# Performance work log

Hardware: AMD Instinct MI355X
Metric: run time of the kernel (lower is better)

Reference implementation:

```python
import jax, jax.numpy as jnp
import numpy as np

W, H = 256, 256          # image width (x) and height (y); image indexed [x, y] like the torch code
N = 8192                 # depth-sorted visible gaussians
TILE = 16                # tile_size default
CHUNK = 128              # gaussians composited per scan step (N % CHUNK == 0)
MIN_WEIGHT = 1e-6        # early-termination threshold from render_pixel


def setup_inputs() -> dict:
    key = jax.random.key(0)
    k1, k2, k3, k4, k5 = jax.random.split(key, 5)
    # pixel-space means, uniformly over the image
    points_xy = jax.random.uniform(k1, (N, 2), dtype=jnp.float32) * jnp.array([W, H], jnp.float32)
    # SPD inverse 2D covariances: Sigma = R diag(var) R^T, inv = R diag(1/var) R^T
    theta = jax.random.uniform(k2, (N,), dtype=jnp.float32) * (2.0 * np.pi)
    sig = jax.random.uniform(k3, (N, 2), dtype=jnp.float32, minval=1.5, maxval=8.0)
    var = sig ** 2
    ct, st = jnp.cos(theta), jnp.sin(theta)
    R = jnp.stack([jnp.stack([ct, -st], -1), jnp.stack([st, ct], -1)], -2)  # [N,2,2]
    inverse_covariance = jnp.einsum('nij,nj,nkj->nik', R, 1.0 / var, R)
    # radius = ceil(2.5 * sqrt(max eigenvalue)) as in compute_radius
    radius = jnp.ceil(2.5 * jnp.sqrt(jnp.max(var, axis=1)))
    colors = jax.random.uniform(k4, (N, 3), dtype=jnp.float32)
    opacity = jax.random.normal(k5, (N,), dtype=jnp.float32)  # pre-sigmoid logits
    return dict(points_xy=points_xy, inverse_covariance=inverse_covariance,
                radius=radius, colors=colors, opacity=opacity)


def _rasterize(points_xy, inverse_covariance, radius, colors, opacity):
    px = jnp.arange(W, dtype=jnp.float32)[:, None]   # [W,1] pixel x coords
    py = jnp.arange(H, dtype=jnp.float32)[None, :]   # [1,H] pixel y coords
    # tile origin for each pixel (tile-based culling as in render_image)
    tile_x0 = ((jnp.arange(W) // TILE) * TILE).astype(jnp.float32)[:, None]  # [W,1]
    tile_y0 = ((jnp.arange(H) // TILE) * TILE).astype(jnp.float32)[None, :]  # [1,H]
    # per-gaussian bounding boxes (preprocess)
    min_x = jnp.floor(points_xy[:, 0] - radius); max_x = jnp.ceil(points_xy[:, 0] + radius)
    min_y = jnp.floor(points_xy[:, 1] - radius); max_y = jnp.ceil(points_xy[:, 1] + radius)

    n_chunks = N // CHUNK
    def chunk(a):
        return a.reshape((n_chunks, CHUNK) + a.shape[1:])
    xs = dict(mx=chunk(points_xy[:, 0]), my=chunk(points_xy[:, 1]),
              a=chunk(inverse_covariance[:, 0, 0]), b=chunk(inverse_covariance[:, 0, 1]),
              c=chunk(inverse_covariance[:, 1, 1]),
              mnx=chunk(min_x), mxx=chunk(max_x), mny=chunk(min_y), mxy=chunk(max_y),
              col=chunk(colors), op=chunk(opacity))

    @jax.checkpoint
    def body(carry, ch):
        T, color = carry  # T: [W,H] remaining transmittance; color: [W,H,3]
        dx = px[None] - ch['mx'][:, None, None]  # [C,W,1]
        dy = py[None] - ch['my'][:, None, None]  # [C,1,H]
        # mahalanobis form d^T Sigma^{-1} d with symmetric inv cov [[a,b],[b,c]]
        q = (ch['a'][:, None, None] * dx * dx
             + 2.0 * ch['b'][:, None, None] * dx * dy
             + ch['c'][:, None, None] * dy * dy)              # [C,W,H]
        alpha = jnp.exp(-0.5 * q) * jax.nn.sigmoid(ch['op'])[:, None, None]
        # gaussian participates for a pixel iff its bbox intersects that pixel's tile
        in_tile = ((ch['mnx'][:, None, None] <= tile_x0[None] + TILE)
                   & (ch['mxx'][:, None, None] >= tile_x0[None])
                   & (ch['mny'][:, None, None] <= tile_y0[None] + TILE)
                   & (ch['mxy'][:, None, None] >= tile_y0[None]))   # [C,W,H]
        alpha = jnp.where(in_tile, alpha, 0.0)
        cum = jnp.cumprod(1.0 - alpha, axis=0)                 # inclusive prefix of (1-alpha)
        T_before = T[None] * jnp.concatenate([jnp.ones_like(cum[:1]), cum[:-1]], axis=0)
        # original: test_weight = T_before*(1-alpha); terminate (skip contribution) if < min_weight
        include = (T[None] * cum) >= MIN_WEIGHT
        contrib = jnp.where(include, T_before * alpha, 0.0)   # [C,W,H]
        color = color + jnp.einsum('cwh,cd->whd', contrib, ch['col'])
        return (T * cum[-1], color), None

    init = (jnp.ones((W, H), jnp.float32), jnp.zeros((W, H, 3), jnp.float32))
    (_, color), _ = jax.lax.scan(body, init, xs)
    return color  # [W,H,3] image indexed [x,y]


def reference(points_xy, inverse_covariance, radius, colors, opacity):
    return _rasterize(points_xy, inverse_covariance, radius, colors, opacity)
```

## Files before the change

### kernel.cpp

```cpp
#include <hip/hip_runtime.h>
#include <hip/hip_fp16.h>

#define WIDTH   256
#define HEIGHT  256
#define NG      8192
#define TILE_SZ 16
#define MINW    1e-6f
#define BLK     1024
#define NBATCH  (NG / BLK)
#define NWAVE   (BLK / 64)
#define NSEG    8
#define PXB     128
#define RSZ     1024

__global__ __launch_bounds__(BLK, 8) void raster_kernel(
    const float* __restrict__ pts,
    const float* __restrict__ icov,
    const float* __restrict__ rad,
    const float* __restrict__ cols,
    const float* __restrict__ opac,
    float* __restrict__ out)
{
    __shared__ unsigned long long s_ball[NBATCH * NWAVE];
    __shared__ int s_pfx[NBATCH * NWAVE];
    __shared__ unsigned short s_list[NG];
    __shared__ float4 s_g[RSZ * 2];
    __shared__ float s_P[NSEG][PXB];
    __shared__ float s_red[NSEG][PXB][3];

    const int tid  = threadIdx.x;
    const int lane = tid & 63;
    const int wave = tid >> 6;
    const int seg  = tid >> 7;
    const int pxl  = tid & (PXB - 1);
    const int px   = blockIdx.z * PXB + pxl;
    const float tx0 = (float)(blockIdx.x * TILE_SZ);
    const float ty0 = (float)(blockIdx.y * TILE_SZ);
    const float tx1 = tx0 + (float)TILE_SZ;
    const float ty1 = ty0 + (float)TILE_SZ;

    unsigned int hitbits = 0;
    for (int b = 0; b < NBATCH; ++b) {
        const int g = b * BLK + tid;
        const float2 p = ((const float2*)pts)[g];
        const float  r = rad[g];
        bool hit = (floorf(p.x - r) <= tx1) & (ceilf(p.x + r) >= tx0)
                 & (floorf(p.y - r) <= ty1) & (ceilf(p.y + r) >= ty0);
        unsigned long long m = __ballot(hit);
        if (lane == 0) s_ball[b * NWAVE + wave] = m;
        if (hit) hitbits |= (1u << b);
    }
    __syncthreads();
    if (wave == 0) {
        int v0 = __popcll(s_ball[lane]);
        int v1 = __popcll(s_ball[64 + lane]);
        #pragma unroll
        for (int d = 1; d < 64; d <<= 1) {
            const int t0 = __shfl_up(v0, d);
            const int t1 = __shfl_up(v1, d);
            if (lane >= d) { v0 += t0; v1 += t1; }
        }
        s_pfx[lane] = v0;
        s_pfx[64 + lane] = v1 + __shfl(v0, 63);
    }
    __syncthreads();
    const int count = s_pfx[127];
    {
        unsigned int hb = hitbits;
        const unsigned long long ltmask = (1ull << lane) - 1ull;
        while (hb) {
            const int b = __ffs(hb) - 1;  hb &= hb - 1;
            const int idx = b * NWAVE + wave;
            const unsigned long long m = s_ball[idx];
            const int bs = idx ? s_pfx[idx - 1] : 0;
            s_list[bs + __popcll(m & ltmask)] = (unsigned short)(b * BLK + tid);
        }
    }
    __syncthreads();

    const float fx = tx0 + (float)(px >> 4);
    const float fy = ty0 + (float)(px & 15);
    const float kc = -0.72134752044f;
    float T = 1.0f, accr = 0.0f, accg = 0.0f, accb = 0.0f;

    for (int base = 0; base < count; base += RSZ) {
        const int n = min(RSZ, count - base);
        if (tid < n) {
            const int g = s_list[base + tid];
            const float2 p = ((const float2*)pts)[g];
            const float4 ic = ((const float4*)icov)[g];
            const float op = 1.0f / (1.0f + __expf(-opac[g]));
            const __half2 h = __floats2half2_rn(cols[3 * g], cols[3 * g + 1]);
            unsigned rgbits; __builtin_memcpy(&rgbits, &h, 4);
            s_g[tid * 2 + 0] = make_float4(p.x, p.y, kc * ic.x, 2.0f * kc * ic.y);
            s_g[tid * 2 + 1] = make_float4(kc * ic.w, op, __uint_as_float(rgbits),
                                           cols[3 * g + 2]);
        }
        __syncthreads();

        const int L = (n + NSEG - 1) >> 3;
        const int i0 = seg * L;
        const int i1 = min(i0 + L, n);

        float P = 1.0f, lr = 0.0f, lg = 0.0f, lb = 0.0f;
        if (__ballot(T >= MINW) != 0ull) {
            #pragma unroll 4
            for (int i = i0; i < i1; ++i) {
                const float4 g0 = s_g[i * 2 + 0];
                const float4 g1 = s_g[i * 2 + 1];
                const float dx = fx - g0.x, dy = fy - g0.y;
                const float q = (g0.z * dx) * dx + (g0.w * dx) * dy + (g1.x * dy) * dy;
                const float a = g1.y * __builtin_amdgcn_exp2f(q);
                const float w = P * a;
                const unsigned rgbits = __float_as_uint(g1.z);
                __half2 h; __builtin_memcpy(&h, &rgbits, 4);
                const float2 rg = __half22float2(h);
                lr = fmaf(w, rg.x, lr);
                lg = fmaf(w, rg.y, lg);
                lb = fmaf(w, g1.w, lb);
                P = fmaf(-a, P, P);
            }
        }
        s_P[seg][pxl] = P;
        __syncthreads();

        float pv[NSEG];
        #pragma unroll
        for (int s = 0; s < NSEG; ++s) pv[s] = s_P[s][pxl];
        float Tin = T, Tnext = T;
        #pragma unroll
        for (int s = 0; s < NSEG; ++s) {
            if (s < seg) Tin *= pv[s];
            Tnext *= pv[s];
        }

        const bool alive = (Tin >= MINW);
        const bool gated = alive && (Tin * P < MINW);
        if (alive && !gated) {
            accr = fmaf(Tin, lr, accr);
            accg = fmaf(Tin, lg, accg);
            accb = fmaf(Tin, lb, accb);
        }
        if (__ballot(gated) != 0ull) {
            float Tl = Tin;
            for (int i = i0; i < i1; ++i) {
                const float4 g0 = s_g[i * 2 + 0];
                const float4 g1 = s_g[i * 2 + 1];
                const float dx = fx - g0.x, dy = fy - g0.y;
                const float q = (g0.z * dx) * dx + (g0.w * dx) * dy + (g1.x * dy) * dy;
                const float a = g1.y * __builtin_amdgcn_exp2f(q);
                const float Tn = Tl * (1.0f - a);
                const float w = (gated && Tn >= MINW) ? Tl * a : 0.0f;
                const unsigned rgbits = __float_as_uint(g1.z);
                __half2 h; __builtin_memcpy(&h, &rgbits, 4);
                const float2 rg = __half22float2(h);
                accr = fmaf(w, rg.x, accr);
                accg = fmaf(w, rg.y, accg);
                accb = fmaf(w, g1.w, accb);
                Tl = Tn;
            }
        }
        T = Tnext;
        if (__syncthreads_count(T < MINW) == BLK) break;
    }

    s_red[seg][pxl][0] = accr;
    s_red[seg][pxl][1] = accg;
    s_red[seg][pxl][2] = accb;
    __syncthreads();
    if (tid < PXB * 3) {
        const int p  = tid / 3;
        const int ch = tid - 3 * p;
        float v = 0.0f;
        #pragma unroll
        for (int s = 0; s < NSEG; ++s) v += s_red[s][p][ch];
        const int pg = blockIdx.z * PXB + p;
        const int x = blockIdx.x * TILE_SZ + (pg >> 4);
        const int y = blockIdx.y * TILE_SZ + (pg & 15);
        out[(x * HEIGHT + y) * 3 + ch] = v;
    }
}

extern "C" void kernel_launch(void* const* d_in, const int* in_sizes, int n_in,
                              void* d_out, int out_size, void* d_ws, size_t ws_size,
                              hipStream_t stream) {
    const float* pts  = (const float*)d_in[0];
    const float* icov = (const float*)d_in[1];
    const float* rad  = (const float*)d_in[2];
    const float* cols = (const float*)d_in[3];
    const float* opac = (const float*)d_in[4];
    float* out = (float*)d_out;
    dim3 grid(WIDTH / TILE_SZ, HEIGHT / TILE_SZ, 2);
    raster_kernel<<<grid, dim3(BLK), 0, stream>>>(pts, icov, rad, cols, opac, out);
}
```

Before: 84.82 us.

## Process two pixels per thread and split gaussians into sixteen segments

Each thread now shades two pixels (four rows apart) per gaussian loaded from shared memory, sharing the dy-dependent terms and the color unpack. The block is therefore split into 16 gaussian segments of one wave each instead of 8 segments of 128 threads. The reduction buffer now aliases the gaussian staging buffer to save LDS. This is meant to halve the shared-memory loads per pixel-gaussian evaluation and reuse the y-terms, at the cost of more registers per thread and a longer serial prefix combine over 16 segments.

```diff
diff --git a/kernel.cpp b/kernel.cpp
--- a/kernel.cpp
+++ b/kernel.cpp
@@ -9,7 +9,7 @@
 #define BLK     1024
 #define NBATCH  (NG / BLK)
 #define NWAVE   (BLK / 64)
-#define NSEG    8
+#define NSEG    16
 #define PXB     128
 #define RSZ     1024
 
@@ -26,14 +26,13 @@
     __shared__ unsigned short s_list[NG];
     __shared__ float4 s_g[RSZ * 2];
     __shared__ float s_P[NSEG][PXB];
-    __shared__ float s_red[NSEG][PXB][3];
+    float* s_red = (float*)s_g;
 
     const int tid  = threadIdx.x;
     const int lane = tid & 63;
     const int wave = tid >> 6;
-    const int seg  = tid >> 7;
-    const int pxl  = tid & (PXB - 1);
-    const int px   = blockIdx.z * PXB + pxl;
+    const int seg  = tid >> 6;
+    const int pair = tid & 63;
     const float tx0 = (float)(blockIdx.x * TILE_SZ);
     const float ty0 = (float)(blockIdx.y * TILE_SZ);
     const float tx1 = tx0 + (float)TILE_SZ;
@@ -78,10 +77,14 @@
     }
     __syncthreads();
 
-    const float fx = tx0 + (float)(px >> 4);
-    const float fy = ty0 + (float)(px & 15);
+    const int pA = pair;
+    const int pB = pair + 64;
+    const float fy  = ty0 + (float)(pair & 15);
+    const float fxA = tx0 + (float)(blockIdx.z * 8 + (pair >> 4));
+    const float fxB = fxA + 4.0f;
     const float kc = -0.72134752044f;
-    float T = 1.0f, accr = 0.0f, accg = 0.0f, accb = 0.0f;
+    float TA = 1.0f, TB = 1.0f;
+    float arA = 0.f, agA = 0.f, abA = 0.f, arB = 0.f, agB = 0.f, abB = 0.f;
 
     for (int base = 0; base < count; base += RSZ) {
         const int n = min(RSZ, count - base);
@@ -98,85 +101,109 @@
         }
         __syncthreads();
 
-        const int L = (n + NSEG - 1) >> 3;
+        const int L  = (n + NSEG - 1) >> 4;
         const int i0 = seg * L;
         const int i1 = min(i0 + L, n);
 
-        float P = 1.0f, lr = 0.0f, lg = 0.0f, lb = 0.0f;
-        if (__ballot(T >= MINW) != 0ull) {
+        float PA = 1.0f, PB = 1.0f;
+        float lrA = 0.f, lgA = 0.f, lbA = 0.f, lrB = 0.f, lgB = 0.f, lbB = 0.f;
+        if (__ballot((TA >= MINW) || (TB >= MINW)) != 0ull) {
             #pragma unroll 4
             for (int i = i0; i < i1; ++i) {
                 const float4 g0 = s_g[i * 2 + 0];
                 const float4 g1 = s_g[i * 2 + 1];
-                const float dx = fx - g0.x, dy = fy - g0.y;
-                const float q = (g0.z * dx) * dx + (g0.w * dx) * dy + (g1.x * dy) * dy;
-                const float a = g1.y * __builtin_amdgcn_exp2f(q);
-                const float w = P * a;
+                const float dy    = fy - g0.y;
+                const float bdy   = g0.w * dy;
+                const float cdydy = (g1.x * dy) * dy;
                 const unsigned rgbits = __float_as_uint(g1.z);
                 __half2 h; __builtin_memcpy(&h, &rgbits, 4);
                 const float2 rg = __half22float2(h);
-                lr = fmaf(w, rg.x, lr);
-                lg = fmaf(w, rg.y, lg);
-                lb = fmaf(w, g1.w, lb);
-                P = fmaf(-a, P, P);
+                const float dxA = fxA - g0.x;
+                const float qA  = fmaf(fmaf(g0.z, dxA, bdy), dxA, cdydy);
+                const float aA  = g1.y * __builtin_amdgcn_exp2f(qA);
+                const float wA  = PA * aA;
+                lrA = fmaf(wA, rg.x, lrA);
+                lgA = fmaf(wA, rg.y, lgA);
+                lbA = fmaf(wA, g1.w, lbA);
+                PA  = fmaf(-aA, PA, PA);
+                const float dxB = fxB - g0.x;
+                const float qB  = fmaf(fmaf(g0.z, dxB, bdy), dxB, cdydy);
+                const float aB  = g1.y * __builtin_amdgcn_exp2f(qB);
+                const float wB  = PB * aB;
+                lrB = fmaf(wB, rg.x, lrB);
+                lgB = fmaf(wB, rg.y, lgB);
+                lbB = fmaf(wB, g1.w, lbB);
+                PB  = fmaf(-aB, PB, PB);
             }
         }
-        s_P[seg][pxl] = P;
+        s_P[seg][pA] = PA;
+        s_P[seg][pB] = PB;
         __syncthreads();
 
-        float pv[NSEG];
-        #pragma unroll
-        for (int s = 0; s < NSEG; ++s) pv[s] = s_P[s][pxl];
-        float Tin = T, Tnext = T;
+        float TinA = TA, TnxA = TA, TinB = TB, TnxB = TB;
         #pragma unroll
         for (int s = 0; s < NSEG; ++s) {
-            if (s < seg) Tin *= pv[s];
-            Tnext *= pv[s];
-        }
-
-        const bool alive = (Tin >= MINW);
-        const bool gated = alive && (Tin * P < MINW);
-        if (alive && !gated) {
-            accr = fmaf(Tin, lr, accr);
-            accg = fmaf(Tin, lg, accg);
-            accb = fmaf(Tin, lb, accb);
-        }
-        if (__ballot(gated) != 0ull) {
-            float Tl = Tin;
+            const float vA = s_P[s][pA];
+            const float vB = s_P[s][pB];
+            if (s < seg) { TinA *= vA; TinB *= vB; }
+            TnxA *= vA;  TnxB *= vB;
+        }
+
+        const bool aliveA = (TinA >= MINW), aliveB = (TinB >= MINW);
+        const bool gatedA = aliveA && (TinA * PA < MINW);
+        const bool gatedB = aliveB && (TinB * PB < MINW);
+        if (aliveA && !gatedA) {
+            arA = fmaf(TinA, lrA, arA); agA = fmaf(TinA, lgA, agA); abA = fmaf(TinA, lbA, abA);
+        }
+        if (aliveB && !gatedB) {
+            arB = fmaf(TinB, lrB, arB); agB = fmaf(TinB, lgB, agB); abB = fmaf(TinB, lbB, abB);
+        }
+        if (__ballot(gatedA || gatedB) != 0ull) {
+            float TlA = TinA, TlB = TinB;
             for (int i = i0; i < i1; ++i) {
                 const float4 g0 = s_g[i * 2 + 0];
                 const float4 g1 = s_g[i * 2 + 1];
-                const float dx = fx - g0.x, dy = fy - g0.y;
-                const float q = (g0.z * dx) * dx + (g0.w * dx) * dy + (g1.x * dy) * dy;
-                const float a = g1.y * __builtin_amdgcn_exp2f(q);
-                const float Tn = Tl * (1.0f - a);
-                const float w = (gated && Tn >= MINW) ? Tl * a : 0.0f;
+                const float dy    = fy - g0.y;
+                const float bdy   = g0.w * dy;
+                const float cdydy = (g1.x * dy) * dy;
                 const unsigned rgbits = __float_as_uint(g1.z);
                 __half2 h; __builtin_memcpy(&h, &rgbits, 4);
                 const float2 rg = __half22float2(h);
-                accr = fmaf(w, rg.x, accr);
-                accg = fmaf(w, rg.y, accg);
-                accb = fmaf(w, g1.w, accb);
-                Tl = Tn;
+                const float dxA = fxA - g0.x;
+                const float aA  = g1.y * __builtin_amdgcn_exp2f(
+                                      fmaf(fmaf(g0.z, dxA, bdy), dxA, cdydy));
+                const float TnA = TlA * (1.0f - aA);
+                const float wA  = (gatedA && TnA >= MINW) ? TlA * aA : 0.0f;
+                arA = fmaf(wA, rg.x, arA); agA = fmaf(wA, rg.y, agA); abA = fmaf(wA, g1.w, abA);
+                TlA = TnA;
+                const float dxB = fxB - g0.x;
+                const float aB  = g1.y * __builtin_amdgcn_exp2f(
+                                      fmaf(fmaf(g0.z, dxB, bdy), dxB, cdydy));
+                const float TnB = TlB * (1.0f - aB);
+                const float wB  = (gatedB && TnB >= MINW) ? TlB * aB : 0.0f;
+                arB = fmaf(wB, rg.x, arB); agB = fmaf(wB, rg.y, agB); abB = fmaf(wB, g1.w, abB);
+                TlB = TnB;
             }
         }
-        T = Tnext;
-        if (__syncthreads_count(T < MINW) == BLK) break;
-    }
-
-    s_red[seg][pxl][0] = accr;
-    s_red[seg][pxl][1] = accg;
-    s_red[seg][pxl][2] = accb;
+        TA = TnxA;  TB = TnxB;
+        if (__syncthreads_count((TA < MINW) && (TB < MINW)) == BLK) break;
+    }
+
+    s_red[seg * (PXB * 3) + pA * 3 + 0] = arA;
+    s_red[seg * (PXB * 3) + pA * 3 + 1] = agA;
+    s_red[seg * (PXB * 3) + pA * 3 + 2] = abA;
+    s_red[seg * (PXB * 3) + pB * 3 + 0] = arB;
+    s_red[seg * (PXB * 3) + pB * 3 + 1] = agB;
+    s_red[seg * (PXB * 3) + pB * 3 + 2] = abB;
     __syncthreads();
     if (tid < PXB * 3) {
+        float v = 0.0f;
+        #pragma unroll
+        for (int s = 0; s < NSEG; ++s) v += s_red[s * (PXB * 3) + tid];
         const int p  = tid / 3;
         const int ch = tid - 3 * p;
-        float v = 0.0f;
-        #pragma unroll
-        for (int s = 0; s < NSEG; ++s) v += s_red[s][p][ch];
-        const int pg = blockIdx.z * PXB + p;
-        const int x = blockIdx.x * TILE_SZ + (pg >> 4);
-        const int y = blockIdx.y * TILE_SZ + (pg & 15);
+        const int x = blockIdx.x * TILE_SZ + blockIdx.z * 8 + (p >> 4);
+        const int y = blockIdx.y * TILE_SZ + (p & 15);
         out[(x * HEIGHT + y) * 3 + ch] = v;
     }
 }
```

After: 83.05 us. 1.02x faster.

## Shrink gaussian staging batch, alias shared buffers, centralize transmittance scan

Applied to the files above, without the earlier changes.

Halves the staging batch to 512 gaussians and aliases the index list, gaussian buffer and reduction buffer into one shared pool to reduce LDS footprint. The per-thread cross-segment transmittance product is replaced by a serial scan done by 128 threads that writes each segment's entry transmittance back to shared memory, at the cost of an extra barrier per batch. The warp-level early-skip ballot on the main loop is removed and the early-exit check now runs only on the first 128 threads. The quadratic form is also rewritten with nested fmas.

```diff
diff --git a/kernel.cpp b/kernel.cpp
--- a/kernel.cpp
+++ b/kernel.cpp
@@ -11,7 +11,8 @@
 #define NWAVE   (BLK / 64)
 #define NSEG    8
 #define PXB     128
-#define RSZ     1024
+#define RSZ     512
+#define KC      (-0.72134752044f)
 
 __global__ __launch_bounds__(BLK, 8) void raster_kernel(
     const float* __restrict__ pts,
@@ -23,23 +24,24 @@
 {
     __shared__ unsigned long long s_ball[NBATCH * NWAVE];
     __shared__ int s_pfx[NBATCH * NWAVE];
-    __shared__ unsigned short s_list[NG];
-    __shared__ float4 s_g[RSZ * 2];
+    __shared__ __align__(16) char s_pool[32768];
+    unsigned short* s_list = (unsigned short*)s_pool;
+    float4* s_g = (float4*)(s_pool + 16384);
+    float*  s_red = (float*)s_pool;
     __shared__ float s_P[NSEG][PXB];
-    __shared__ float s_red[NSEG][PXB][3];
 
     const int tid  = threadIdx.x;
     const int lane = tid & 63;
     const int wave = tid >> 6;
     const int seg  = tid >> 7;
-    const int pxl  = tid & (PXB - 1);
-    const int px   = blockIdx.z * PXB + pxl;
+    const int px   = tid & (PXB - 1);
     const float tx0 = (float)(blockIdx.x * TILE_SZ);
     const float ty0 = (float)(blockIdx.y * TILE_SZ);
     const float tx1 = tx0 + (float)TILE_SZ;
     const float ty1 = ty0 + (float)TILE_SZ;
 
     unsigned int hitbits = 0;
+    #pragma unroll
     for (int b = 0; b < NBATCH; ++b) {
         const int g = b * BLK + tid;
         const float2 p = ((const float2*)pts)[g];
@@ -78,10 +80,10 @@
     }
     __syncthreads();
 
-    const float fx = tx0 + (float)(px >> 4);
+    const float fx = tx0 + (float)(blockIdx.z * 8 + (px >> 4));
     const float fy = ty0 + (float)(px & 15);
-    const float kc = -0.72134752044f;
-    float T = 1.0f, accr = 0.0f, accg = 0.0f, accb = 0.0f;
+    float Tpx = 1.0f;
+    float ar = 0.f, ag = 0.f, ab = 0.f;
 
     for (int base = 0; base < count; base += RSZ) {
         const int n = min(RSZ, count - base);
@@ -92,91 +94,98 @@
             const float op = 1.0f / (1.0f + __expf(-opac[g]));
             const __half2 h = __floats2half2_rn(cols[3 * g], cols[3 * g + 1]);
             unsigned rgbits; __builtin_memcpy(&rgbits, &h, 4);
-            s_g[tid * 2 + 0] = make_float4(p.x, p.y, kc * ic.x, 2.0f * kc * ic.y);
-            s_g[tid * 2 + 1] = make_float4(kc * ic.w, op, __uint_as_float(rgbits),
+            s_g[tid * 2 + 0] = make_float4(p.x, p.y, KC * ic.x, 2.0f * KC * ic.y);
+            s_g[tid * 2 + 1] = make_float4(KC * ic.w, op, __uint_as_float(rgbits),
                                            cols[3 * g + 2]);
         }
         __syncthreads();
 
-        const int L = (n + NSEG - 1) >> 3;
+        const int L  = (n + NSEG - 1) >> 3;
         const int i0 = seg * L;
         const int i1 = min(i0 + L, n);
 
-        float P = 1.0f, lr = 0.0f, lg = 0.0f, lb = 0.0f;
-        if (__ballot(T >= MINW) != 0ull) {
-            #pragma unroll 4
-            for (int i = i0; i < i1; ++i) {
-                const float4 g0 = s_g[i * 2 + 0];
-                const float4 g1 = s_g[i * 2 + 1];
-                const float dx = fx - g0.x, dy = fy - g0.y;
-                const float q = (g0.z * dx) * dx + (g0.w * dx) * dy + (g1.x * dy) * dy;
-                const float a = g1.y * __builtin_amdgcn_exp2f(q);
-                const float w = P * a;
-                const unsigned rgbits = __float_as_uint(g1.z);
-                __half2 h; __builtin_memcpy(&h, &rgbits, 4);
-                const float2 rg = __half22float2(h);
-                lr = fmaf(w, rg.x, lr);
-                lg = fmaf(w, rg.y, lg);
-                lb = fmaf(w, g1.w, lb);
-                P = fmaf(-a, P, P);
+        float P = 1.0f, lr = 0.f, lg = 0.f, lb = 0.f;
+        #pragma unroll 4
+        for (int i = i0; i < i1; ++i) {
+            const float4 g0 = s_g[i * 2 + 0];
+            const float4 g1 = s_g[i * 2 + 1];
+            const float dx = fx - g0.x;
+            const float dy = fy - g0.y;
+            const float q  = fmaf(dx, fmaf(g0.z, dx, g0.w * dy),
+                                  (g1.x * dy) * dy);
+            const float a  = g1.y * __builtin_amdgcn_exp2f(q);
+            const float w  = P * a;
+            const unsigned rgbits = __float_as_uint(g1.z);
+            __half2 h; __builtin_memcpy(&h, &rgbits, 4);
+            const float2 rg = __half22float2(h);
+            lr = fmaf(w, rg.x, lr);
+            lg = fmaf(w, rg.y, lg);
+            lb = fmaf(w, g1.w, lb);
+            P  = fmaf(-a, P, P);
+        }
+        s_P[seg][px] = P;
+        __syncthreads();
+
+        if (tid < PXB) {
+            float run = Tpx;
+            #pragma unroll
+            for (int s = 0; s < NSEG; ++s) {
+                const float Pv = s_P[s][tid];
+                s_P[s][tid] = run;
+                run *= Pv;
             }
-        }
-        s_P[seg][pxl] = P;
+            Tpx = run;
+        }
         __syncthreads();
 
-        float pv[NSEG];
-        #pragma unroll
-        for (int s = 0; s < NSEG; ++s) pv[s] = s_P[s][pxl];
-        float Tin = T, Tnext = T;
-        #pragma unroll
-        for (int s = 0; s < NSEG; ++s) {
-            if (s < seg) Tin *= pv[s];
-            Tnext *= pv[s];
-        }
-
+        const float Tin  = s_P[seg][px];
         const bool alive = (Tin >= MINW);
         const bool gated = alive && (Tin * P < MINW);
         if (alive && !gated) {
-            accr = fmaf(Tin, lr, accr);
-            accg = fmaf(Tin, lg, accg);
-            accb = fmaf(Tin, lb, accb);
+            ar = fmaf(Tin, lr, ar);
+            ag = fmaf(Tin, lg, ag);
+            ab = fmaf(Tin, lb, ab);
         }
         if (__ballot(gated) != 0ull) {
             float Tl = Tin;
             for (int i = i0; i < i1; ++i) {
                 const float4 g0 = s_g[i * 2 + 0];
                 const float4 g1 = s_g[i * 2 + 1];
-                const float dx = fx - g0.x, dy = fy - g0.y;
-                const float q = (g0.z * dx) * dx + (g0.w * dx) * dy + (g1.x * dy) * dy;
-                const float a = g1.y * __builtin_amdgcn_exp2f(q);
+                const float dx = fx - g0.x;
+                const float dy = fy - g0.y;
+                const float q  = fmaf(dx, fmaf(g0.z, dx, g0.w * dy),
+                                      (g1.x * dy) * dy);
+                const float a  = g1.y * __builtin_amdgcn_exp2f(q);
                 const float Tn = Tl * (1.0f - a);
-                const float w = (gated && Tn >= MINW) ? Tl * a : 0.0f;
+                const float w  = (gated && Tn >= MINW) ? Tl * a : 0.0f;
                 const unsigned rgbits = __float_as_uint(g1.z);
                 __half2 h; __builtin_memcpy(&h, &rgbits, 4);
                 const float2 rg = __half22float2(h);
-                accr = fmaf(w, rg.x, accr);
-                accg = fmaf(w, rg.y, accg);
-                accb = fmaf(w, g1.w, accb);
+                ar = fmaf(w, rg.x, ar);
+                ag = fmaf(w, rg.y, ag);
+                ab = fmaf(w, g1.w, ab);
                 Tl = Tn;
             }
         }
-        T = Tnext;
-        if (__syncthreads_count(T < MINW) == BLK) break;
-    }
-
-    s_red[seg][pxl][0] = accr;
-    s_red[seg][pxl][1] = accg;
-    s_red[seg][pxl][2] = accb;
+        if (base + RSZ < count) {
+            const bool mydead = (tid < PXB) ? (Tpx < MINW) : true;
+            if (__syncthreads_count(mydead) == BLK) break;
+        }
+    }
+    __syncthreads();
+
+    s_red[(seg * PXB + px) * 3 + 0] = ar;
+    s_red[(seg * PXB + px) * 3 + 1] = ag;
+    s_red[(seg * PXB + px) * 3 + 2] = ab;
     __syncthreads();
     if (tid < PXB * 3) {
         const int p  = tid / 3;
         const int ch = tid - 3 * p;
         float v = 0.0f;
         #pragma unroll
-        for (int s = 0; s < NSEG; ++s) v += s_red[s][p][ch];
-        const int pg = blockIdx.z * PXB + p;
-        const int x = blockIdx.x * TILE_SZ + (pg >> 4);
-        const int y = blockIdx.y * TILE_SZ + (pg & 15);
+        for (int s = 0; s < NSEG; ++s) v += s_red[(s * PXB + p) * 3 + ch];
+        const int x = blockIdx.x * TILE_SZ + blockIdx.z * 8 + (p >> 4);
+        const int y = blockIdx.y * TILE_SZ + (p & 15);
         out[(x * HEIGHT + y) * 3 + ch] = v;
     }
 }
```

Measured after the change: 81.99 us. 1.03x faster.
